# Kernel optimization log

Measured on AMD Instinct MI355X. Metric: run time of the kernel, lower is better.

The kernel has to match this reference:

```python
import jax, jax.numpy as jnp
import numpy as np

NUM_GRAPHS = 64
NEG_SLOPE = 0.2


def _gatv2_layer(x, src, dst, edge_attr, Wl, Wr, We, att, b):
    """PyG GATv2Conv (heads=1) with self-loops (fill_value='mean')."""
    n = x.shape[0]
    # self-loop edge_attr = mean of incoming edge_attr per target node
    ones = jnp.ones((src.shape[0],), dtype=x.dtype)
    deg = jax.ops.segment_sum(ones, dst, num_segments=n)
    ea_sum = jax.ops.segment_sum(edge_attr, dst, num_segments=n)
    loop_attr = ea_sum / jnp.maximum(deg, 1.0)[:, None]
    loop = jnp.arange(n)
    src_f = jnp.concatenate([src, loop])
    dst_f = jnp.concatenate([dst, loop])
    ea_f = jnp.concatenate([edge_attr, loop_attr], axis=0)

    xl = x @ Wl              # source transform [N, out]
    xr = x @ Wr              # target transform [N, out]
    ee = ea_f @ We           # edge transform   [E+N, out]

    m = xl[src_f] + xr[dst_f] + ee                      # [E+N, out]
    m = jax.nn.leaky_relu(m, NEG_SLOPE)
    s = m @ att                                         # [E+N] attention logits

    # segment softmax over incoming edges of each target node
    smax = jax.ops.segment_max(s, dst_f, num_segments=n)
    e = jnp.exp(s - smax[dst_f])
    denom = jax.ops.segment_sum(e, dst_f, num_segments=n)
    alpha = e / (denom[dst_f] + 1e-16)

    out = jax.ops.segment_sum(alpha[:, None] * xl[src_f], dst_f, num_segments=n)
    return out + b


def setup_inputs() -> dict:
    key = jax.random.key(0)
    ks = jax.random.split(key, 16)
    N, E, D, ED = 50000, 640000, 128, 16
    sc = 0.1
    inp = {
        "node_features": jax.random.normal(ks[0], (N, D), jnp.float32),
        "edge_index": jax.random.randint(ks[1], (2, E), 0, N, jnp.int64),
        "batch": jnp.sort(jax.random.randint(ks[2], (N,), 0, 64, jnp.int64)),
        "edge_attr": jax.random.normal(ks[3], (E, ED), jnp.float32),
        "Wl1": jax.random.normal(ks[4], (D, D), jnp.float32) * sc,
        "Wr1": jax.random.normal(ks[5], (D, D), jnp.float32) * sc,
        "We1": jax.random.normal(ks[6], (ED, D), jnp.float32) * sc,
        "att1": jax.random.normal(ks[7], (D,), jnp.float32) * sc,
        "b1": jnp.zeros((D,), jnp.float32),
        "Wl2": jax.random.normal(ks[8], (D, D), jnp.float32) * sc,
        "Wr2": jax.random.normal(ks[9], (D, D), jnp.float32) * sc,
        "We2": jax.random.normal(ks[10], (ED, D), jnp.float32) * sc,
        "att2": jax.random.normal(ks[11], (D,), jnp.float32) * sc,
        "b2": jnp.zeros((D,), jnp.float32),
    }
    return inp


def reference(node_features, edge_index, batch, edge_attr,
              Wl1, Wr1, We1, att1, b1, Wl2, Wr2, We2, att2, b2):
    src, dst = edge_index[0], edge_index[1]
    x = _gatv2_layer(node_features, src, dst, edge_attr, Wl1, Wr1, We1, att1, b1)
    x = jax.nn.relu(x)
    x = _gatv2_layer(x, src, dst, edge_attr, Wl2, Wr2, We2, att2, b2)
    x = jax.nn.relu(x)
    # global mean pool over the full node set (node_subset_indices defaults to arange)
    cnt = jax.ops.segment_sum(jnp.ones((x.shape[0],), x.dtype), batch, num_segments=NUM_GRAPHS)
    pooled = jax.ops.segment_sum(x, batch, num_segments=NUM_GRAPHS)
    return pooled / jnp.maximum(cnt, 1.0)[:, None]
```

## Files before the change

kernel.cpp:

```cpp
#include <hip/hip_runtime.h>
#include <hip/hip_bf16.h>
#include <math.h>

#define D 128
#define ED 16
#define NUM_GRAPHS 64
#define SCAN_CHUNK 2048


__global__ void deg_kernel(const int* __restrict__ dst, int* __restrict__ deg, int E) {
  int e = blockIdx.x * 256 + threadIdx.x;
  if (e < E) atomicAdd(&deg[dst[e]], 1);
}

__global__ __launch_bounds__(256) void scan_reduce_kernel(const int* __restrict__ deg,
                                                          int* __restrict__ bsum, int N) {
  int b = blockIdx.x, tid = threadIdx.x;
  int base = b * SCAN_CHUNK + tid * 8;
  int s = 0;
#pragma unroll
  for (int j = 0; j < 8; ++j) {
    int idx = base + j;
    if (idx < N) s += deg[idx];
  }
#pragma unroll
  for (int off = 1; off < 64; off <<= 1) s += __shfl_xor(s, off);
  __shared__ int ws[4];
  int lane = tid & 63, w = tid >> 6;
  if (lane == 0) ws[w] = s;
  __syncthreads();
  if (tid == 0) bsum[b] = ws[0] + ws[1] + ws[2] + ws[3];
}

__global__ void scan_bsum_kernel(const int* __restrict__ bsum, int* __restrict__ boff,
                                 int* __restrict__ rowptrN, int B) {
  int tid = threadIdx.x;
  int v = (tid < B) ? bsum[tid] : 0;
  int x = v;
#pragma unroll
  for (int off = 1; off < 64; off <<= 1) {
    int y = __shfl_up(x, off);
    if (tid >= off) x += y;
  }
  if (tid < B) boff[tid] = x - v;
  if (tid == 63) *rowptrN = x;
}

__global__ __launch_bounds__(256) void scan_write_kernel(const int* __restrict__ deg,
                                                         const int* __restrict__ boff,
                                                         int* __restrict__ rowptr, int N) {
  int b = blockIdx.x, tid = threadIdx.x;
  int lane = tid & 63, w = tid >> 6;
  int base = b * SCAN_CHUNK + tid * 8;
  int v[8];
  int s = 0;
#pragma unroll
  for (int j = 0; j < 8; ++j) {
    int idx = base + j;
    v[j] = (idx < N) ? deg[idx] : 0;
    s += v[j];
  }
  int t = s, x = t;
#pragma unroll
  for (int off = 1; off < 64; off <<= 1) {
    int y = __shfl_up(x, off);
    if (lane >= off) x += y;
  }
  __shared__ int wsum[4];
  if (lane == 63) wsum[w] = x;
  __syncthreads();
  int wexc = 0;
  for (int i = 0; i < w; ++i) wexc += wsum[i];
  int run = boff[b] + wexc + (x - t);
#pragma unroll
  for (int j = 0; j < 8; ++j) {
    int idx = base + j;
    if (idx < N) rowptr[idx] = run;
    run += v[j];
  }
}

__global__ void scatter_kernel(const int* __restrict__ src, const int* __restrict__ dst,
                               const int* __restrict__ rowptr, int* __restrict__ cursor,
                               int2* __restrict__ csr, int E) {
  int e = blockIdx.x * 256 + threadIdx.x;
  if (e >= E) return;
  int d = dst[e];
  int pos = rowptr[d] + atomicAdd(&cursor[d], 1);
  csr[pos] = make_int2(src[e], e);
}


__global__ __launch_bounds__(256) void gemm2_kernel(const float* __restrict__ x,
                                                    const float* __restrict__ Wl,
                                                    const float* __restrict__ Wr,
                                                    float* __restrict__ xl,
                                                    float* __restrict__ xr, int N) {
  __shared__ float xst[D][64];
  __shared__ float ws[16][256];
  int tid = threadIdx.x;
  int base = blockIdx.x * 64;

#pragma unroll
  for (int j = 0; j < 8; ++j) {
    int idx = tid + j * 256;
    int row = idx & 63;
    int c4 = idx >> 6;
    int n = base + row;
    float4 v = make_float4(0.f, 0.f, 0.f, 0.f);
    if (n < N) v = *(const float4*)&x[(size_t)n * D + c4 * 4];
    xst[c4 * 4 + 0][row] = v.x;
    xst[c4 * 4 + 1][row] = v.y;
    xst[c4 * 4 + 2][row] = v.z;
    xst[c4 * 4 + 3][row] = v.w;
  }

  int tn = tid & 15;
  int tc = tid >> 4;
  float acc[4][16];
#pragma unroll
  for (int i = 0; i < 4; ++i)
#pragma unroll
    for (int j = 0; j < 16; ++j) acc[i][j] = 0.f;

  for (int kb = 0; kb < D; kb += 16) {
    __syncthreads();
#pragma unroll
    for (int j = 0; j < 4; ++j) {
      int idx = tid + j * 256;
      int c4 = idx & 63;
      int kk = idx >> 6;
      int c = c4 * 4;
      const float* Wp = (c < D) ? &Wl[(size_t)(kb + kk) * D + c]
                                : &Wr[(size_t)(kb + kk) * D + (c - D)];
      *(float4*)&ws[kk][c] = *(const float4*)Wp;
    }
    __syncthreads();
#pragma unroll
    for (int kk = 0; kk < 16; ++kk) {
      float4 xv = *(float4*)&xst[kb + kk][tn * 4];
      float xa[4] = {xv.x, xv.y, xv.z, xv.w};
      float4 w0 = *(float4*)&ws[kk][tc * 16 + 0];
      float4 w1 = *(float4*)&ws[kk][tc * 16 + 4];
      float4 w2 = *(float4*)&ws[kk][tc * 16 + 8];
      float4 w3 = *(float4*)&ws[kk][tc * 16 + 12];
      float wa[16] = {w0.x, w0.y, w0.z, w0.w, w1.x, w1.y, w1.z, w1.w,
                      w2.x, w2.y, w2.z, w2.w, w3.x, w3.y, w3.z, w3.w};
#pragma unroll
      for (int i = 0; i < 4; ++i)
#pragma unroll
        for (int j = 0; j < 16; ++j) acc[i][j] = fmaf(xa[i], wa[j], acc[i][j]);
    }
  }

#pragma unroll
  for (int i = 0; i < 4; ++i) {
    int n = base + tn * 4 + i;
    if (n >= N) continue;
    float* outp;
    int c;
    if (tc < 8) { outp = xl; c = tc * 16; }
    else        { outp = xr; c = (tc - 8) * 16; }
#pragma unroll
    for (int j4 = 0; j4 < 4; ++j4) {
      float4 v = make_float4(acc[i][j4 * 4 + 0], acc[i][j4 * 4 + 1],
                             acc[i][j4 * 4 + 2], acc[i][j4 * 4 + 3]);
      *(float4*)&outp[(size_t)n * D + c + j4 * 4] = v;
    }
  }
}


__global__ __launch_bounds__(256) void gat_fused_kernel(
    const float* __restrict__ xl, const float* __restrict__ xr,
    const int* __restrict__ rowptr, const int2* __restrict__ csr,
    const float* __restrict__ ea, const float* __restrict__ We,
    const float* __restrict__ att, const float* __restrict__ bias,
    float* __restrict__ y, int N, int nwaves) {
  __shared__ float ea_lds[4][4][16];
  int lane = threadIdx.x & 63;
  int wid = threadIdx.x >> 6;
  int gwave = blockIdx.x * 4 + wid;

  float weL[ED], weH[ED];
#pragma unroll
  for (int k = 0; k < ED; ++k) {
    float2 w = *(const float2*)&We[k * D + 2 * lane];
    weL[k] = w.x;
    weH[k] = w.y;
  }
  float2 attv = *(const float2*)&att[2 * lane];
  float2 bv = *(const float2*)&bias[2 * lane];

  int ej = lane >> 4;
  int ek = lane & 15;

  for (int n = gwave; n < N; n += nwaves) {
    float2 xrv = *(const float2*)&xr[(size_t)n * D + 2 * lane];
    float2 xsl = *(const float2*)&xl[(size_t)n * D + 2 * lane];
    int beg = rowptr[n], end = rowptr[n + 1];

    float denom = 0.f, acc0 = 0.f, acc1 = 0.f, easum = 0.f;

    for (int i = beg; i < end; i += 4) {
      int cnt = end - i;
      int last = end - 1;
      int i1 = (i + 1 < end) ? i + 1 : last;
      int i2 = (i + 2 < end) ? i + 2 : last;
      int i3 = (i + 3 < end) ? i + 3 : last;
      int2 c0 = csr[i], c1 = csr[i1], c2 = csr[i2], c3 = csr[i3];

      float2 xs0 = *(const float2*)&xl[(size_t)c0.x * D + 2 * lane];
      float2 xs1 = *(const float2*)&xl[(size_t)c1.x * D + 2 * lane];
      float2 xs2 = *(const float2*)&xl[(size_t)c2.x * D + 2 * lane];
      float2 xs3 = *(const float2*)&xl[(size_t)c3.x * D + 2 * lane];

      int eidj = (ej == 0) ? c0.y : (ej == 1) ? c1.y : (ej == 2) ? c2.y : c3.y;
      float a = ea[(size_t)eidj * ED + ek];
      ea_lds[wid][ej][ek] = a;
      easum += (ej < cnt) ? a : 0.f;

      float pre[4];
      float2 xsa[4] = {xs0, xs1, xs2, xs3};
#pragma unroll
      for (int j = 0; j < 4; ++j) {
        const float4* eap = (const float4*)&ea_lds[wid][j][0];
        float4 q0 = eap[0], q1 = eap[1], q2 = eap[2], q3 = eap[3];
        float av[16] = {q0.x, q0.y, q0.z, q0.w, q1.x, q1.y, q1.z, q1.w,
                        q2.x, q2.y, q2.z, q2.w, q3.x, q3.y, q3.z, q3.w};
        float e0 = 0.f, e1 = 0.f;
#pragma unroll
        for (int k = 0; k < ED; ++k) {
          e0 = fmaf(av[k], weL[k], e0);
          e1 = fmaf(av[k], weH[k], e1);
        }
        float t0 = xsa[j].x + xrv.x + e0;
        t0 = (t0 > 0.f) ? t0 : 0.2f * t0;
        float t1 = xsa[j].y + xrv.y + e1;
        t1 = (t1 > 0.f) ? t1 : 0.2f * t1;
        pre[j] = fmaf(t0, attv.x, t1 * attv.y);
      }

#pragma unroll
      for (int off = 32; off > 0; off >>= 1) {
#pragma unroll
        for (int j = 0; j < 4; ++j) pre[j] += __shfl_xor(pre[j], off);
      }

#pragma unroll
      for (int j = 0; j < 4; ++j) {
        float w = (j < cnt) ? __expf(pre[j]) : 0.f;
        denom += w;
        acc0 = fmaf(w, xsa[j].x, acc0);
        acc1 = fmaf(w, xsa[j].y, acc1);
      }
    }

    easum += __shfl_xor(easum, 16);
    easum += __shfl_xor(easum, 32);
    float dg = fmaxf((float)(end - beg), 1.0f);
    if (ej == 0) ea_lds[wid][0][ek] = easum / dg;
    {
      const float4* eap = (const float4*)&ea_lds[wid][0][0];
      float4 q0 = eap[0], q1 = eap[1], q2 = eap[2], q3 = eap[3];
      float av[16] = {q0.x, q0.y, q0.z, q0.w, q1.x, q1.y, q1.z, q1.w,
                      q2.x, q2.y, q2.z, q2.w, q3.x, q3.y, q3.z, q3.w};
      float e0 = 0.f, e1 = 0.f;
#pragma unroll
      for (int k = 0; k < ED; ++k) {
        e0 = fmaf(av[k], weL[k], e0);
        e1 = fmaf(av[k], weH[k], e1);
      }
      float t0 = xsl.x + xrv.x + e0;
      t0 = (t0 > 0.f) ? t0 : 0.2f * t0;
      float t1 = xsl.y + xrv.y + e1;
      t1 = (t1 > 0.f) ? t1 : 0.2f * t1;
      float p = fmaf(t0, attv.x, t1 * attv.y);
#pragma unroll
      for (int off = 32; off > 0; off >>= 1) p += __shfl_xor(p, off);
      float w = __expf(p);
      denom += w;
      acc0 = fmaf(w, xsl.x, acc0);
      acc1 = fmaf(w, xsl.y, acc1);
    }

    float inv = 1.0f / (denom + 1e-16f);
    float o0 = fmaxf(fmaf(acc0, inv, bv.x), 0.f);
    float o1 = fmaxf(fmaf(acc1, inv, bv.y), 0.f);
    *(float2*)&y[(size_t)n * D + 2 * lane] = make_float2(o0, o1);
  }
}


__global__ __launch_bounds__(128) void pool_kernel(const float* __restrict__ y,
                                                   const int* __restrict__ batch,
                                                   float* __restrict__ out, int N) {
  int g = blockIdx.x;
  int part = blockIdx.y;
  int d = threadIdx.x;
  __shared__ int se[2];
  if (d < 2) {
    int target = g + d;
    int lo = 0, hi = N;
    while (lo < hi) {
      int mid = (lo + hi) >> 1;
      if (batch[mid] < target) lo = mid + 1;
      else hi = mid;
    }
    se[d] = lo;
  }
  __syncthreads();
  int start = se[0], end = se[1];
  int len = end - start;
  int q = (len + 3) >> 2;
  int ps = start + part * q;
  int pe = min(ps + q, end);
  float s0 = 0.f, s1 = 0.f, s2 = 0.f, s3 = 0.f;
  int nn = ps;
  for (; nn + 3 < pe; nn += 4) {
    s0 += y[(size_t)(nn + 0) * D + d];
    s1 += y[(size_t)(nn + 1) * D + d];
    s2 += y[(size_t)(nn + 2) * D + d];
    s3 += y[(size_t)(nn + 3) * D + d];
  }
  for (; nn < pe; ++nn) s0 += y[(size_t)nn * D + d];
  float sum = (s0 + s1) + (s2 + s3);
  float cnt = fmaxf((float)len, 1.0f);
  if (ps < pe) atomicAdd(&out[g * D + d], sum / cnt);
  else if (part == 0 && len <= 0) out[g * D + d] = 0.f;
}


static inline size_t alignup(size_t v) { return (v + 255) & ~(size_t)255; }

extern "C" void kernel_launch(void* const* d_in, const int* in_sizes, int n_in,
                              void* d_out, int out_size, void* d_ws, size_t ws_size,
                              hipStream_t stream) {
  const float* xnode = (const float*)d_in[0];
  const int* eidx = (const int*)d_in[1];
  const int* batch = (const int*)d_in[2];
  const float* eattr = (const float*)d_in[3];
  const float* Wl1 = (const float*)d_in[4];
  const float* Wr1 = (const float*)d_in[5];
  const float* We1 = (const float*)d_in[6];
  const float* att1 = (const float*)d_in[7];
  const float* b1 = (const float*)d_in[8];
  const float* Wl2 = (const float*)d_in[9];
  const float* Wr2 = (const float*)d_in[10];
  const float* We2 = (const float*)d_in[11];
  const float* att2 = (const float*)d_in[12];
  const float* b2 = (const float*)d_in[13];
  float* out = (float*)d_out;

  int N = in_sizes[0] / D;
  int E = in_sizes[3] / ED;
  const int* srcp = eidx;
  const int* dstp = eidx + E;
  int B = (N + SCAN_CHUNK - 1) / SCAN_CHUNK;

  char* p = (char*)d_ws;
  int* rowptr = (int*)p;    p += alignup((size_t)(N + 1) * 4);
  int* deg = (int*)p;       p += alignup((size_t)N * 4);
  int* cursor = (int*)p;    p += alignup((size_t)N * 4);
  int* bsum = (int*)p;      p += alignup((size_t)B * 4);
  int* boff = (int*)p;      p += alignup((size_t)B * 4);
  int2* csr = (int2*)p;     p += alignup((size_t)E * 8);
  float* xlb = (float*)p;   p += alignup((size_t)N * D * 4);
  float* xrb = (float*)p;   p += alignup((size_t)N * D * 4);
  float* yb = (float*)p;    p += alignup((size_t)N * D * 4);

  hipMemsetAsync(deg, 0, (size_t)N * 4, stream);
  hipMemsetAsync(cursor, 0, (size_t)N * 4, stream);
  hipMemsetAsync(out, 0, (size_t)NUM_GRAPHS * D * 4, stream);

  deg_kernel<<<(E + 255) / 256, 256, 0, stream>>>(dstp, deg, E);
  scan_reduce_kernel<<<B, 256, 0, stream>>>(deg, bsum, N);
  scan_bsum_kernel<<<1, 64, 0, stream>>>(bsum, boff, rowptr + N, B);
  scan_write_kernel<<<B, 256, 0, stream>>>(deg, boff, rowptr, N);
  scatter_kernel<<<(E + 255) / 256, 256, 0, stream>>>(srcp, dstp, rowptr, cursor, csr, E);

  int gblocks = 2048;
  int nwaves = gblocks * 4;

  gemm2_kernel<<<(N + 63) / 64, 256, 0, stream>>>(xnode, Wl1, Wr1, xlb, xrb, N);
  gat_fused_kernel<<<gblocks, 256, 0, stream>>>(xlb, xrb, rowptr, csr, eattr,
                                                We1, att1, b1, yb, N, nwaves);
  gemm2_kernel<<<(N + 63) / 64, 256, 0, stream>>>(yb, Wl2, Wr2, xlb, xrb, N);
  gat_fused_kernel<<<gblocks, 256, 0, stream>>>(xlb, xrb, rowptr, csr, eattr,
                                                We2, att2, b2, yb, N, nwaves);
  dim3 pgrid(NUM_GRAPHS, 4);
  pool_kernel<<<pgrid, 128, 0, stream>>>(yb, batch, out, N);

  (void)ws_size; (void)n_in; (void)out_size;
}
```

Baseline: 610.9 us.

## Fuse degree count into first GEMM, pooling into final GAT, drop cursor memset

Degree counting now runs as extra blocks of the first GEMM launch, so the two overlap instead of running back to back. The per-graph inverse counts are computed in the scan-bsum kernel. The final GAT layer atomically accumulates scaled outputs straight into the pooled result, which removes the y write-back and the separate pool kernel. The scan now initialises the cursor with row offsets, which drops one memset and a rowptr load in scatter. The cost is many float atomics on only 64 graph rows in the last layer, which may contend heavily and makes the summation order non-deterministic.

```diff
diff --git a/kernel.cpp b/kernel.cpp
--- a/kernel.cpp
+++ b/kernel.cpp
@@ -7,11 +7,6 @@
 #define NUM_GRAPHS 64
 #define SCAN_CHUNK 2048
 
-
-__global__ void deg_kernel(const int* __restrict__ dst, int* __restrict__ deg, int E) {
-  int e = blockIdx.x * 256 + threadIdx.x;
-  if (e < E) atomicAdd(&deg[dst[e]], 1);
-}
 
 __global__ __launch_bounds__(256) void scan_reduce_kernel(const int* __restrict__ deg,
                                                           int* __restrict__ bsum, int N) {
@@ -33,7 +28,9 @@
 }
 
 __global__ void scan_bsum_kernel(const int* __restrict__ bsum, int* __restrict__ boff,
-                                 int* __restrict__ rowptrN, int B) {
+                                 int* __restrict__ rowptrN, int B,
+                                 const int* __restrict__ batch, float* __restrict__ ginv,
+                                 int N) {
   int tid = threadIdx.x;
   int v = (tid < B) ? bsum[tid] : 0;
   int x = v;
@@ -44,11 +41,23 @@
   }
   if (tid < B) boff[tid] = x - v;
   if (tid == 63) *rowptrN = x;
+
+  int lo = 0, hi = N;
+  while (lo < hi) {
+    int mid = (lo + hi) >> 1;
+    if (batch[mid] < tid) lo = mid + 1;
+    else hi = mid;
+  }
+  int startg = lo;
+  int nxt = __shfl_down(startg, 1);
+  if (tid == 63) nxt = N;
+  if (tid < NUM_GRAPHS) ginv[tid] = 1.0f / fmaxf((float)(nxt - startg), 1.0f);
 }
 
 __global__ __launch_bounds__(256) void scan_write_kernel(const int* __restrict__ deg,
                                                          const int* __restrict__ boff,
-                                                         int* __restrict__ rowptr, int N) {
+                                                         int* __restrict__ rowptr,
+                                                         int* __restrict__ cursor, int N) {
   int b = blockIdx.x, tid = threadIdx.x;
   int lane = tid & 63, w = tid >> 6;
   int base = b * SCAN_CHUNK + tid * 8;
@@ -75,30 +84,42 @@
 #pragma unroll
   for (int j = 0; j < 8; ++j) {
     int idx = base + j;
-    if (idx < N) rowptr[idx] = run;
+    if (idx < N) {
+      rowptr[idx] = run;
+      cursor[idx] = run;
+    }
     run += v[j];
   }
 }
 
 __global__ void scatter_kernel(const int* __restrict__ src, const int* __restrict__ dst,
-                               const int* __restrict__ rowptr, int* __restrict__ cursor,
-                               int2* __restrict__ csr, int E) {
+                               int* __restrict__ cursor, int2* __restrict__ csr, int E) {
   int e = blockIdx.x * 256 + threadIdx.x;
   if (e >= E) return;
   int d = dst[e];
-  int pos = rowptr[d] + atomicAdd(&cursor[d], 1);
+  int pos = atomicAdd(&cursor[d], 1);
   csr[pos] = make_int2(src[e], e);
 }
 
 
-__global__ __launch_bounds__(256) void gemm2_kernel(const float* __restrict__ x,
-                                                    const float* __restrict__ Wl,
-                                                    const float* __restrict__ Wr,
-                                                    float* __restrict__ xl,
-                                                    float* __restrict__ xr, int N) {
+__global__ __launch_bounds__(256) void gemm2_deg_kernel(const float* __restrict__ x,
+                                                        const float* __restrict__ Wl,
+                                                        const float* __restrict__ Wr,
+                                                        float* __restrict__ xl,
+                                                        float* __restrict__ xr, int N,
+                                                        const int* __restrict__ dstp,
+                                                        int* __restrict__ deg, int E,
+                                                        int gB) {
   __shared__ float xst[D][64];
   __shared__ float ws[16][256];
   int tid = threadIdx.x;
+
+  if (blockIdx.x >= gB) {
+    int e = (blockIdx.x - gB) * 256 + tid;
+    if (e < E) atomicAdd(&deg[dstp[e]], 1);
+    return;
+  }
+
   int base = blockIdx.x * 64;
 
 #pragma unroll
@@ -171,12 +192,14 @@
 }
 
 
+template <bool FINAL>
 __global__ __launch_bounds__(256) void gat_fused_kernel(
     const float* __restrict__ xl, const float* __restrict__ xr,
     const int* __restrict__ rowptr, const int2* __restrict__ csr,
     const float* __restrict__ ea, const float* __restrict__ We,
     const float* __restrict__ att, const float* __restrict__ bias,
-    float* __restrict__ y, int N, int nwaves) {
+    float* __restrict__ y, const int* __restrict__ batch,
+    const float* __restrict__ ginv, float* __restrict__ out, int N, int nwaves) {
   __shared__ float ea_lds[4][4][16];
   int lane = threadIdx.x & 63;
   int wid = threadIdx.x >> 6;
@@ -287,47 +310,15 @@
     float inv = 1.0f / (denom + 1e-16f);
     float o0 = fmaxf(fmaf(acc0, inv, bv.x), 0.f);
     float o1 = fmaxf(fmaf(acc1, inv, bv.y), 0.f);
-    *(float2*)&y[(size_t)n * D + 2 * lane] = make_float2(o0, o1);
-  }
-}
-
-
-__global__ __launch_bounds__(128) void pool_kernel(const float* __restrict__ y,
-                                                   const int* __restrict__ batch,
-                                                   float* __restrict__ out, int N) {
-  int g = blockIdx.x;
-  int part = blockIdx.y;
-  int d = threadIdx.x;
-  __shared__ int se[2];
-  if (d < 2) {
-    int target = g + d;
-    int lo = 0, hi = N;
-    while (lo < hi) {
-      int mid = (lo + hi) >> 1;
-      if (batch[mid] < target) lo = mid + 1;
-      else hi = mid;
-    }
-    se[d] = lo;
-  }
-  __syncthreads();
-  int start = se[0], end = se[1];
-  int len = end - start;
-  int q = (len + 3) >> 2;
-  int ps = start + part * q;
-  int pe = min(ps + q, end);
-  float s0 = 0.f, s1 = 0.f, s2 = 0.f, s3 = 0.f;
-  int nn = ps;
-  for (; nn + 3 < pe; nn += 4) {
-    s0 += y[(size_t)(nn + 0) * D + d];
-    s1 += y[(size_t)(nn + 1) * D + d];
-    s2 += y[(size_t)(nn + 2) * D + d];
-    s3 += y[(size_t)(nn + 3) * D + d];
-  }
-  for (; nn < pe; ++nn) s0 += y[(size_t)nn * D + d];
-  float sum = (s0 + s1) + (s2 + s3);
-  float cnt = fmaxf((float)len, 1.0f);
-  if (ps < pe) atomicAdd(&out[g * D + d], sum / cnt);
-  else if (part == 0 && len <= 0) out[g * D + d] = 0.f;
+    if (FINAL) {
+      int g = batch[n];
+      float sc = ginv[g];
+      atomicAdd(&out[(size_t)g * D + 2 * lane], o0 * sc);
+      atomicAdd(&out[(size_t)g * D + 2 * lane + 1], o1 * sc);
+    } else {
+      *(float2*)&y[(size_t)n * D + 2 * lane] = make_float2(o0, o1);
+    }
+  }
 }
 
 
@@ -364,32 +355,35 @@
   int* cursor = (int*)p;    p += alignup((size_t)N * 4);
   int* bsum = (int*)p;      p += alignup((size_t)B * 4);
   int* boff = (int*)p;      p += alignup((size_t)B * 4);
+  float* ginv = (float*)p;  p += alignup((size_t)NUM_GRAPHS * 4);
   int2* csr = (int2*)p;     p += alignup((size_t)E * 8);
   float* xlb = (float*)p;   p += alignup((size_t)N * D * 4);
   float* xrb = (float*)p;   p += alignup((size_t)N * D * 4);
   float* yb = (float*)p;    p += alignup((size_t)N * D * 4);
 
   hipMemsetAsync(deg, 0, (size_t)N * 4, stream);
-  hipMemsetAsync(cursor, 0, (size_t)N * 4, stream);
   hipMemsetAsync(out, 0, (size_t)NUM_GRAPHS * D * 4, stream);
 
-  deg_kernel<<<(E + 255) / 256, 256, 0, stream>>>(dstp, deg, E);
-  scan_reduce_kernel<<<B, 256, 0, stream>>>(deg, bsum, N);
-  scan_bsum_kernel<<<1, 64, 0, stream>>>(bsum, boff, rowptr + N, B);
-  scan_write_kernel<<<B, 256, 0, stream>>>(deg, boff, rowptr, N);
-  scatter_kernel<<<(E + 255) / 256, 256, 0, stream>>>(srcp, dstp, rowptr, cursor, csr, E);
-
+  int gB = (N + 63) / 64;
+  int degB = (E + 255) / 256;
   int gblocks = 2048;
   int nwaves = gblocks * 4;
 
-  gemm2_kernel<<<(N + 63) / 64, 256, 0, stream>>>(xnode, Wl1, Wr1, xlb, xrb, N);
-  gat_fused_kernel<<<gblocks, 256, 0, stream>>>(xlb, xrb, rowptr, csr, eattr,
-                                                We1, att1, b1, yb, N, nwaves);
-  gemm2_kernel<<<(N + 63) / 64, 256, 0, stream>>>(yb, Wl2, Wr2, xlb, xrb, N);
-  gat_fused_kernel<<<gblocks, 256, 0, stream>>>(xlb, xrb, rowptr, csr, eattr,
-                                                We2, att2, b2, yb, N, nwaves);
-  dim3 pgrid(NUM_GRAPHS, 4);
-  pool_kernel<<<pgrid, 128, 0, stream>>>(yb, batch, out, N);
+  gemm2_deg_kernel<<<gB + degB, 256, 0, stream>>>(xnode, Wl1, Wr1, xlb, xrb, N,
+                                                  dstp, deg, E, gB);
+  scan_reduce_kernel<<<B, 256, 0, stream>>>(deg, bsum, N);
+  scan_bsum_kernel<<<1, 64, 0, stream>>>(bsum, boff, rowptr + N, B, batch, ginv, N);
+  scan_write_kernel<<<B, 256, 0, stream>>>(deg, boff, rowptr, cursor, N);
+  scatter_kernel<<<degB, 256, 0, stream>>>(srcp, dstp, cursor, csr, E);
+
+  gat_fused_kernel<false><<<gblocks, 256, 0, stream>>>(
+      xlb, xrb, rowptr, csr, eattr, We1, att1, b1, yb, nullptr, nullptr, nullptr,
+      N, nwaves);
+  gemm2_deg_kernel<<<gB, 256, 0, stream>>>(yb, Wl2, Wr2, xlb, xrb, N,
+                                           nullptr, nullptr, 0, gB);
+  gat_fused_kernel<true><<<gblocks, 256, 0, stream>>>(
+      xlb, xrb, rowptr, csr, eattr, We2, att2, b2, nullptr, batch, ginv, out,
+      N, nwaves);
 
   (void)ws_size; (void)n_in; (void)out_size;
 }
```

Result: slower. 675.2 us (+10.5%).
